# Kernel tuning notes

Hardware: AMD Instinct MI355X
Metric: run time of the kernel (lower is better)

Reference implementation:

```python
import jax, jax.numpy as jnp
import numpy as np

BATCH, SEQ, DIM, HEADS, DSTATE, BLOCK = 2, 4096, 1024, 16, 64, 64
LN_EPS = 1e-6

def segsum(x):
    # x: (..., T) -> (..., T, T); segsum[i, j] = sum_{j < k <= i} x[k]; -inf above diagonal
    T = x.shape[-1]
    cs = jnp.cumsum(x, axis=-1)
    seg = cs[..., :, None] - cs[..., None, :]
    mask = jnp.tril(jnp.ones((T, T), dtype=bool))
    return jnp.where(mask, seg, -jnp.inf)

def ssd_minimal_discrete(X, A, C, B, block_len):
    # X: (b,s,h,p) already multiplied by dt; A: (b,s,h) = A*dt; C readout, B input: (b,s,h,n)
    b, s, h, p = X.shape
    n = B.shape[-1]
    c = s // block_len
    l = block_len
    Xc = X.reshape(b, c, l, h, p)
    Bc = B.reshape(b, c, l, h, n)
    Cc = C.reshape(b, c, l, h, n)
    Ac = A.reshape(b, c, l, h).transpose(0, 3, 1, 2)  # (b,h,c,l)
    A_cumsum = jnp.cumsum(Ac, axis=-1)
    # 1. intra-chunk (diagonal block) outputs
    L = jnp.exp(segsum(Ac))  # (b,h,c,l,l)
    Y_diag = jnp.einsum('bclhn,bcshn,bhcls,bcshp->bclhp', Cc, Bc, L, Xc)
    # 2. states at end of each chunk
    decay_states = jnp.exp(A_cumsum[..., -1:] - A_cumsum)
    states = jnp.einsum('bclhn,bhcl,bclhp->bchpn', Bc, decay_states, Xc)
    # 3. inter-chunk recurrence on chunk states
    init = jnp.zeros_like(states[:, :1])
    states = jnp.concatenate([init, states], axis=1)  # (b,c+1,h,p,n)
    decay_chunk = jnp.exp(segsum(jnp.pad(A_cumsum[..., -1], ((0, 0), (0, 0), (1, 0)))))
    new_states = jnp.einsum('bhzc,bchpn->bzhpn', decay_chunk, states)
    states, final_state = new_states[:, :-1], new_states[:, -1]
    # 4. state -> output contribution (off-diagonal blocks)
    state_decay_out = jnp.exp(A_cumsum)
    Y_off = jnp.einsum('bclhn,bchpn,bhcl->bclhp', Cc, states, state_decay_out)
    return (Y_diag + Y_off).reshape(b, s, h, p), final_state

def setup_inputs():
    key = jax.random.key(0)
    ks = jax.random.split(key, 8)
    X = jax.random.normal(ks[0], (BATCH, SEQ, DIM), jnp.float32)
    B = jax.random.normal(ks[1], (BATCH, SEQ, HEADS * DSTATE), jnp.float32)
    C = jax.random.normal(ks[2], (BATCH, SEQ, HEADS * DSTATE), jnp.float32)
    W_dt = jax.random.normal(ks[3], (DIM, HEADS), jnp.float32) * 0.02
    # dt_bias initializer: inverse-softplus of dt ~ LogUniform(1e-3, 1e-1)
    dt = jnp.exp(jax.random.uniform(ks[4], (1, SEQ, HEADS)) * (jnp.log(0.1) - jnp.log(0.001)) + jnp.log(0.001))
    dt = jnp.clip(dt, 1e-4)
    dt_bias = dt + jnp.log(-jnp.expm1(-dt))
    # a_log initializer: log of Uniform(1, 16)
    a_log = jnp.log(jax.random.uniform(ks[5], (HEADS,), minval=1.0, maxval=16.0))
    W_out = jax.random.normal(ks[6], (DIM, DIM), jnp.float32) * 0.02
    ln_scale = jnp.ones((DIM,), jnp.float32)
    ln_bias = jnp.zeros((DIM,), jnp.float32)
    return {"X": X, "B": B, "C": C, "W_dt": W_dt, "dt_bias": dt_bias, "a_log": a_log,
            "W_out": W_out, "ln_scale": ln_scale, "ln_bias": ln_bias, "block_len": BLOCK}

def reference(X, B, C, W_dt, dt_bias, a_log, W_out, ln_scale, ln_bias, block_len):
    b, s, dim = X.shape
    h = a_log.shape[0]
    Xh = X.reshape(b, s, h, -1)
    Bh = B.reshape(b, s, h, -1)
    Ch = C.reshape(b, s, h, -1)
    dt = jax.nn.softplus(jnp.einsum('bsd,dh->bsh', X, W_dt) + dt_bias)  # (b,s,h)
    A = -jnp.exp(a_log)  # (h,)
    y, final_state = ssd_minimal_discrete(Xh * dt[..., None], A * dt, Ch, Bh, block_len)
    y = y.reshape(b, s, dim)
    mu = jnp.mean(y, axis=-1, keepdims=True)
    var = jnp.mean(jnp.square(y - mu), axis=-1, keepdims=True)
    yn = (y - mu) / jnp.sqrt(var + LN_EPS) * ln_scale + ln_bias
    out = jnp.einsum('bsd,de->bse', yn, W_out)
    return out, final_state
```

## Files before the change

kernel.cpp:

```cpp
#include <hip/hip_runtime.h>
#include <hip/hip_bf16.h>
#include <hip/hip_fp16.h>
#include <math.h>

#define BATCH   2
#define SEQ     4096
#define DIM     1024
#define HEADS   16
#define DSTATE  64
#define HEADDIM 64
#define BLOCKL  64
#define NCHUNK  64
#define ROWS    (BATCH*SEQ)

typedef __attribute__((ext_vector_type(4))) float f32x4;
typedef __attribute__((ext_vector_type(8))) short bf16x8;
typedef __attribute__((ext_vector_type(8))) _Float16 f16x8;

static __device__ __forceinline__ float softplus_f(float x){
    return (x > 20.f) ? x : log1pf(__expf(x));
}
static __device__ __forceinline__ ushort f2b(float f){
    __hip_bfloat16 h = __float2bfloat16(f);
    return *reinterpret_cast<ushort*>(&h);
}
static __device__ __forceinline__ float b2f(ushort u){
    uint x = ((uint)u) << 16;
    return *reinterpret_cast<float*>(&x);
}
static __device__ __forceinline__ void gload16(const void* g, void* l){
    __builtin_amdgcn_global_load_lds((const __attribute__((address_space(1))) unsigned int*)g,
                                     (__attribute__((address_space(3))) unsigned int*)l, 16, 0, 0);
}

__global__ __launch_bounds__(256) void k_dtwt(const float* __restrict__ X,
        const float* __restrict__ Wdt, const float* __restrict__ dtb,
        const float* __restrict__ alog, const float* __restrict__ W,
        float* __restrict__ dt_g, float* __restrict__ dtA_g,
        ushort* __restrict__ Wt){
    __shared__ float xrow[DIM];
    __shared__ float red[16][17];
    __shared__ float t[64][65];
    int bidx = blockIdx.x;
    int tid = threadIdx.x;
    if (bidx < ROWS){
        int r = bidx;
        int s = r & (SEQ-1);
        *(f32x4*)(xrow + tid*4) = *(const f32x4*)(X + (size_t)r*DIM + tid*4);
        __syncthreads();
        int part = tid >> 4, h = tid & 15;
        int d0 = part * 64;
        float acc = 0.f;
        #pragma unroll 8
        for (int i = 0; i < 64; ++i)
            acc += xrow[d0 + i] * Wdt[(size_t)(d0 + i)*HEADS + h];
        red[part][h] = acc;
        __syncthreads();
        if (tid < 16){
            float sum = 0.f;
            #pragma unroll
            for (int p = 0; p < 16; ++p) sum += red[p][tid];
            sum += dtb[(size_t)s*HEADS + tid];
            float dtv = softplus_f(sum);
            dt_g[(size_t)r*HEADS + tid]  = dtv;
            dtA_g[(size_t)r*HEADS + tid] = -__expf(alog[tid]) * dtv;
        }
    } else {
        int bid = bidx - ROWS;
        int kt = bid >> 4, nt = bid & 15;
        int lr = tid >> 4, lc4 = (tid & 15) * 4;
        #pragma unroll
        for (int q = 0; q < 4; ++q){
            int k = lr + q*16;
            *(f32x4*)&t[k][lc4] = *(const f32x4*)(W + (size_t)(kt*64 + k)*DIM + nt*64 + lc4);
        }
        __syncthreads();
        #pragma unroll
        for (int q = 0; q < 4; ++q){
            int n = lr + q*16;
            ushort o[4];
            #pragma unroll
            for (int j = 0; j < 4; ++j) o[j] = f2b(t[lc4+j][n]);
            *(short4*)(Wt + (size_t)(nt*64 + n)*DIM + kt*64 + lc4) = *(short4*)&o[0];
        }
    }
}

__global__ __launch_bounds__(256) void k_chunk(const float* __restrict__ X,
        const float* __restrict__ Bin, const float* __restrict__ Cin,
        const float* __restrict__ dt_g, const float* __restrict__ dtA_g,
        ushort* __restrict__ ybf, ushort* __restrict__ cstate, float* __restrict__ css_g){
    int bid = blockIdx.x;
    int h = bid & 15, c = (bid >> 4) & 63, b = bid >> 10;
    int tid = threadIdx.x;
    int lane = tid & 63, wave = tid >> 6;
    int r0 = b*SEQ + c*BLOCKL;

    __shared__ __align__(16) char region0[18432];
    ushort* Cs  = (ushort*)region0;
    ushort* Bs  = (ushort*)(region0 + 9216);
    ushort* XdT = (ushort*)region0;
    ushort* WBT = (ushort*)(region0 + 9216);
    ushort* Mb  = (ushort*)(region0 + 9216);

    int l  = tid >> 2;
    int c0 = (tid & 3) * 16;

    f32x4 xr[4], br[4], cr[4];
    {
        const float* xp = X   + (size_t)(r0 + l)*DIM + h*HEADDIM + c0;
        const float* bp = Bin + (size_t)(r0 + l)*DIM + h*DSTATE  + c0;
        const float* cp = Cin + (size_t)(r0 + l)*DIM + h*DSTATE  + c0;
        #pragma unroll
        for (int q = 0; q < 4; ++q){
            xr[q] = *(const f32x4*)(xp + q*4);
            br[q] = *(const f32x4*)(bp + q*4);
            cr[q] = *(const f32x4*)(cp + q*4);
        }
    }
    float dt_l = dt_g[(size_t)(r0 + lane)*HEADS + h];
    float a    = dtA_g[(size_t)(r0 + lane)*HEADS + h];
    #pragma unroll
    for (int off = 1; off < 64; off <<= 1){
        float v = __shfl_up(a, off, 64);
        if (lane >= off) a += v;
    }
    float cs63 = __shfl(a, 63, 64);
    float w_l  = __expf(cs63 - a);
    if (tid < 64) css_g[(size_t)bid*64 + tid] = a;

    {
        ushort tc[16], tb[16];
        #pragma unroll
        for (int q = 0; q < 4; ++q)
            #pragma unroll
            for (int j = 0; j < 4; ++j){
                tc[q*4+j] = f2b(cr[q][j]);
                tb[q*4+j] = f2b(br[q][j]);
            }
        *(uint4*)&Cs[l*72 + c0]     = *(uint4*)&tc[0];
        *(uint4*)&Cs[l*72 + c0 + 8] = *(uint4*)&tc[8];
        *(uint4*)&Bs[l*72 + c0]     = *(uint4*)&tb[0];
        *(uint4*)&Bs[l*72 + c0 + 8] = *(uint4*)&tb[8];
    }
    __syncthreads();

    int cl15  = lane & 15;
    int g     = lane >> 4;
    int arow  = wave*16 + cl15;
    int kof   = g * 8;
    int rbase = wave*16 + g*4;

    f32x4 gacc[4];
    #pragma unroll
    for (int j = 0; j < 4; ++j) gacc[j] = (f32x4){0.f,0.f,0.f,0.f};
    #pragma unroll
    for (int k = 0; k < 2; ++k){
        bf16x8 aa = *(const bf16x8*)&Cs[arow*72 + k*32 + kof];
        #pragma unroll
        for (int j = 0; j < 4; ++j){
            bf16x8 bb = *(const bf16x8*)&Bs[(16*j + cl15)*72 + k*32 + kof];
            gacc[j] = __builtin_amdgcn_mfma_f32_16x16x32_bf16(aa, bb, gacc[j], 0, 0, 0);
        }
    }
    __syncthreads();

    {
        float dl = __shfl(dt_l, l, 64);
        float wl = __shfl(w_l,  l, 64);
        #pragma unroll
        for (int q = 0; q < 4; ++q)
            #pragma unroll
            for (int j = 0; j < 4; ++j){
                int p = c0 + q*4 + j;
                XdT[p*72 + l] = f2b(xr[q][j] * dl);
                WBT[p*72 + l] = f2b(br[q][j] * wl);
            }
    }
    __syncthreads();

    f32x4 st[4];
    #pragma unroll
    for (int j = 0; j < 4; ++j) st[j] = (f32x4){0.f,0.f,0.f,0.f};
    #pragma unroll
    for (int k = 0; k < 2; ++k){
        bf16x8 aw = *(const bf16x8*)&XdT[arow*72 + k*32 + kof];
        #pragma unroll
        for (int j = 0; j < 4; ++j){
            bf16x8 bb = *(const bf16x8*)&WBT[(16*j + cl15)*72 + k*32 + kof];
            st[j] = __builtin_amdgcn_mfma_f32_16x16x32_bf16(aw, bb, st[j], 0, 0, 0);
        }
    }
    #pragma unroll
    for (int j = 0; j < 4; ++j)
        #pragma unroll
        for (int r = 0; r < 4; ++r){
            __half hv = __float2half(st[j][r]);
            cstate[(size_t)bid*4096 + (size_t)(rbase + r)*64 + 16*j + cl15] = *(ushort*)&hv;
        }

    float mreg[4][4];
    {
        float csr[4], csc[4];
        #pragma unroll
        for (int r = 0; r < 4; ++r) csr[r] = __shfl(a, rbase + r, 64);
        #pragma unroll
        for (int j = 0; j < 4; ++j) csc[j] = __shfl(a, 16*j + cl15, 64);
        #pragma unroll
        for (int j = 0; j < 4; ++j)
            #pragma unroll
            for (int r = 0; r < 4; ++r){
                int row = rbase + r, col = 16*j + cl15;
                mreg[j][r] = (col <= row) ? gacc[j][r]*__expf(csr[r] - csc[j]) : 0.f;
            }
    }
    __syncthreads();

    #pragma unroll
    for (int j = 0; j < 4; ++j)
        #pragma unroll
        for (int r = 0; r < 4; ++r)
            Mb[(rbase + r)*72 + 16*j + cl15] = f2b(mreg[j][r]);
    __syncthreads();

    f32x4 y[4];
    #pragma unroll
    for (int j = 0; j < 4; ++j) y[j] = (f32x4){0.f,0.f,0.f,0.f};
    #pragma unroll
    for (int k = 0; k < 2; ++k){
        bf16x8 am = *(const bf16x8*)&Mb[arow*72 + k*32 + kof];
        #pragma unroll
        for (int j = 0; j < 4; ++j){
            bf16x8 bx = *(const bf16x8*)&XdT[(16*j + cl15)*72 + k*32 + kof];
            y[j] = __builtin_amdgcn_mfma_f32_16x16x32_bf16(am, bx, y[j], 0, 0, 0);
        }
    }
    #pragma unroll
    for (int j = 0; j < 4; ++j)
        #pragma unroll
        for (int r = 0; r < 4; ++r)
            ybf[(size_t)(r0 + rbase + r)*DIM + h*HEADDIM + 16*j + cl15] = f2b(y[j][r]);
}

__global__ __launch_bounds__(256) void k_scan(ushort* __restrict__ cstate,
        const float* __restrict__ css_g, float* __restrict__ fs_out){
    int bid = blockIdx.x;
    int tile = bid & 7, hh = (bid >> 3) & 15, b = bid >> 7;
    int tid = threadIdx.x;
    int pn = tile*512 + tid*2;
    size_t base0 = (size_t)(b*NCHUNK)*HEADS + hh;
    __shared__ float esh[64];
    if (tid < 64)
        esh[tid] = __expf(css_g[(base0 + (size_t)tid*HEADS)*64 + 63]);
    __syncthreads();
    ushort* p0 = cstate + base0*4096 + pn;
    const size_t cstep = (size_t)HEADS*4096;
    float P0 = 0.f, P1 = 0.f;
    __half2 cur = *(const __half2*)p0;
    __half2 nxt = *(const __half2*)(p0 + cstep);
    for (int c = 0; c < NCHUNK; ++c){
        __half2 fut = nxt;
        if (c + 2 < NCHUNK) fut = *(const __half2*)(p0 + (size_t)(c+2)*cstep);
        *( __half2*)(p0 + (size_t)c*cstep) = __floats2half2_rn(P0, P1);
        float2 cf = __half22float2(cur);
        float e = esh[c];
        P0 = e*P0 + cf.x;
        P1 = e*P1 + cf.y;
        cur = nxt;
        nxt = fut;
    }
    *(float2*)&fs_out[(size_t)(b*HEADS + hh)*4096 + pn] = make_float2(P0, P1);
}

__global__ __launch_bounds__(256) void k_yoff(const float* __restrict__ Cin,
        const ushort* __restrict__ cstate, const float* __restrict__ css_g,
        ushort* __restrict__ ybf){
    int bid = blockIdx.x;
    int h = bid & 15, c = (bid >> 4) & 63, b = bid >> 10;
    int tid = threadIdx.x;
    int lane = tid & 63, wave = tid >> 6;
    int r0 = b*SEQ + c*BLOCKL;
    __shared__ __align__(16) ushort Cs[64*72];
    __shared__ __align__(16) ushort Ss[64*72];
    __shared__ float cse[64];
    {
        int l  = tid >> 2;
        int c0 = (tid & 3) * 16;
        const float* cp = Cin + (size_t)(r0 + l)*DIM + h*DSTATE + c0;
        ushort tc[16];
        #pragma unroll
        for (int q = 0; q < 4; ++q){
            f32x4 vc = *(const f32x4*)(cp + q*4);
            #pragma unroll
            for (int j = 0; j < 4; ++j){
                __half hv = __float2half(vc[j]);
                tc[q*4+j] = *(ushort*)&hv;
            }
        }
        *(uint4*)&Cs[l*72 + c0]     = *(uint4*)&tc[0];
        *(uint4*)&Cs[l*72 + c0 + 8] = *(uint4*)&tc[8];
        const ushort* sp = cstate + (size_t)bid*4096 + (size_t)l*64 + c0;
        *(uint4*)&Ss[l*72 + c0]     = *(const uint4*)sp;
        *(uint4*)&Ss[l*72 + c0 + 8] = *(const uint4*)(sp + 8);
    }
    if (tid < 64) cse[tid] = __expf(css_g[(size_t)bid*64 + tid]);
    __syncthreads();

    int cl15 = lane & 15;
    int g    = lane >> 4;
    int arow = wave*16 + cl15;
    int kof  = g * 8;
    f32x4 acc[4];
    #pragma unroll
    for (int j = 0; j < 4; ++j) acc[j] = (f32x4){0.f,0.f,0.f,0.f};
    #pragma unroll
    for (int k = 0; k < 2; ++k){
        f16x8 a = *(const f16x8*)&Cs[arow*72 + k*32 + kof];
        #pragma unroll
        for (int j = 0; j < 4; ++j){
            f16x8 bb = *(const f16x8*)&Ss[(16*j + cl15)*72 + k*32 + kof];
            acc[j] = __builtin_amdgcn_mfma_f32_16x16x32_f16(a, bb, acc[j], 0, 0, 0);
        }
    }
    int rbase = wave*16 + g*4;
    #pragma unroll
    for (int j = 0; j < 4; ++j)
        #pragma unroll
        for (int r = 0; r < 4; ++r){
            float e = cse[rbase + r];
            size_t idx = (size_t)(r0 + rbase + r)*DIM + h*HEADDIM + 16*j + cl15;
            ybf[idx] = f2b(b2f(ybf[idx]) + e * acc[j][r]);
        }
}

__global__ __launch_bounds__(256) void k_ln(ushort* __restrict__ ybf,
        const float* __restrict__ scale, const float* __restrict__ bias){
    int r = blockIdx.x, tid = threadIdx.x;
    ushort* yp = ybf + (size_t)r*DIM + tid*4;
    short4 raw = *(const short4*)yp;
    float v[4];
    v[0] = b2f((ushort)raw.x); v[1] = b2f((ushort)raw.y);
    v[2] = b2f((ushort)raw.z); v[3] = b2f((ushort)raw.w);
    float s1 = v[0]+v[1]+v[2]+v[3];
    float s2 = v[0]*v[0]+v[1]*v[1]+v[2]*v[2]+v[3]*v[3];
    #pragma unroll
    for (int m = 32; m > 0; m >>= 1){
        s1 += __shfl_xor(s1, m, 64);
        s2 += __shfl_xor(s2, m, 64);
    }
    __shared__ float w1[4], w2[4];
    int wv = tid >> 6;
    if ((tid & 63) == 0){ w1[wv] = s1; w2[wv] = s2; }
    __syncthreads();
    float S1 = w1[0]+w1[1]+w1[2]+w1[3];
    float S2 = w2[0]+w2[1]+w2[2]+w2[3];
    float mu  = S1 * (1.f/DIM);
    float var = S2 * (1.f/DIM) - mu*mu;
    float rstd = rsqrtf(var + 1e-6f);
    int d = tid*4;
    f32x4 sc = *(const f32x4*)(scale + d);
    f32x4 bi = *(const f32x4*)(bias + d);
    ushort o[4];
    #pragma unroll
    for (int j = 0; j < 4; ++j)
        o[j] = f2b((v[j] - mu)*rstd*sc[j] + bi[j]);
    *(short4*)yp = *(short4*)&o[0];
}

__global__ __launch_bounds__(256) void k_gemm(const ushort* __restrict__ A,
        const ushort* __restrict__ Bt, float* __restrict__ Out){
    __shared__ __align__(16) ushort As[128*32];
    __shared__ __align__(16) ushort Bsh[128*32];
    int bid = blockIdx.x;
    int wgid = (bid & 7)*64 + (bid >> 3);
    int bn = wgid & 7, bm = wgid >> 3;
    int tid = threadIdx.x;
    int lane = tid & 63, wave = tid >> 6;
    int wr = wave >> 1, wc = wave & 1;
    f32x4 acc[4][4];
    #pragma unroll
    for (int i = 0; i < 4; ++i)
        #pragma unroll
        for (int j = 0; j < 4; ++j)
            acc[i][j] = (f32x4){0.f, 0.f, 0.f, 0.f};
    const ushort* Ag = A  + (size_t)bm*128*1024;
    const ushort* Bg = Bt + (size_t)bn*128*1024;
    int row0 = tid >> 2;
    int col0 = (tid & 3) * 8;
    for (int k0 = 0; k0 < 1024; k0 += 32){
        const ushort* sA = Ag + (size_t)row0*1024 + k0 + col0;
        const ushort* sB = Bg + (size_t)row0*1024 + k0 + col0;
        gload16(sA,           &As[row0*32 + col0]);
        gload16(sA + 64*1024, &As[(row0+64)*32 + col0]);
        gload16(sB,           &Bsh[row0*32 + col0]);
        gload16(sB + 64*1024, &Bsh[(row0+64)*32 + col0]);
        __syncthreads();
        bf16x8 af[4], bfr[4];
        #pragma unroll
        for (int i = 0; i < 4; ++i){
            int arow = wr*64 + i*16 + (lane & 15);
            af[i] = *(const bf16x8*)&As[arow*32 + ((lane >> 4) << 3)];
        }
        #pragma unroll
        for (int j = 0; j < 4; ++j){
            int brow = wc*64 + j*16 + (lane & 15);
            bfr[j] = *(const bf16x8*)&Bsh[brow*32 + ((lane >> 4) << 3)];
        }
        #pragma unroll
        for (int i = 0; i < 4; ++i)
            #pragma unroll
            for (int j = 0; j < 4; ++j)
                acc[i][j] = __builtin_amdgcn_mfma_f32_16x16x32_bf16(af[i], bfr[j], acc[i][j], 0, 0, 0);
        __syncthreads();
    }
    #pragma unroll
    for (int i = 0; i < 4; ++i){
        int m0 = bm*128 + wr*64 + i*16 + ((lane >> 4) << 2);
        #pragma unroll
        for (int j = 0; j < 4; ++j){
            int n = bn*128 + wc*64 + j*16 + (lane & 15);
            #pragma unroll
            for (int reg = 0; reg < 4; ++reg)
                Out[(size_t)(m0 + reg)*1024 + n] = acc[i][j][reg];
        }
    }
}

extern "C" void kernel_launch(void* const* d_in, const int* in_sizes, int n_in,
                              void* d_out, int out_size, void* d_ws, size_t ws_size,
                              hipStream_t stream){
    const float* X    = (const float*)d_in[0];
    const float* Bin  = (const float*)d_in[1];
    const float* Cin  = (const float*)d_in[2];
    const float* Wdt  = (const float*)d_in[3];
    const float* dtb  = (const float*)d_in[4];
    const float* alog = (const float*)d_in[5];
    const float* Wout = (const float*)d_in[6];
    const float* lns  = (const float*)d_in[7];
    const float* lnb  = (const float*)d_in[8];

    float* out = (float*)d_out;
    float* fs_out = out + (size_t)ROWS*DIM;

    char* ws = (char*)d_ws;
    float*  dt_g   = (float*)(ws);
    float*  dtA_g  = (float*)(ws + 524288);
    float*  css_g  = (float*)(ws + 1048576);
    ushort* cstate = (ushort*)(ws + 1572864);
    ushort* ybf    = (ushort*)(ws + 18350080);
    ushort* Wt     = (ushort*)(ws + 35127296);

    k_dtwt <<<ROWS + 256,         256, 0, stream>>>(X, Wdt, dtb, alog, Wout, dt_g, dtA_g, Wt);
    k_chunk<<<BATCH*NCHUNK*HEADS, 256, 0, stream>>>(X, Bin, Cin, dt_g, dtA_g, ybf, cstate, css_g);
    k_scan <<<BATCH*HEADS*8,      256, 0, stream>>>(cstate, css_g, fs_out);
    k_yoff <<<BATCH*NCHUNK*HEADS, 256, 0, stream>>>(Cin, cstate, css_g, ybf);
    k_ln   <<<ROWS,               256, 0, stream>>>(ybf, lns, lnb);
    k_gemm <<<512,                256, 0, stream>>>(ybf, Wt, out);
}
```

Before: 122.7 us.

## Fuse LayerNorm into output GEMM A-tile load

Removes the standalone LayerNorm kernel. The GEMM now computes per-row mean and rstd for its 128-row A tile in a prologue and normalizes A elements on the fly while staging them into shared memory. This saves one kernel launch and a full read+write pass over the bf16 activations. In exchange, each of the 8 column blocks recomputes the row statistics, which re-reads A, and the A load becomes a register path instead of a direct global-to-LDS load. The result also changes slightly because of when bf16 rounding happens.

Result: slower. 150.4 us (+22.6%).

```diff
diff --git a/kernel.cpp b/kernel.cpp
--- a/kernel.cpp
+++ b/kernel.cpp
@@ -333,67 +333,89 @@
         }
 }
 
-__global__ __launch_bounds__(256) void k_ln(ushort* __restrict__ ybf,
-        const float* __restrict__ scale, const float* __restrict__ bias){
-    int r = blockIdx.x, tid = threadIdx.x;
-    ushort* yp = ybf + (size_t)r*DIM + tid*4;
-    short4 raw = *(const short4*)yp;
-    float v[4];
-    v[0] = b2f((ushort)raw.x); v[1] = b2f((ushort)raw.y);
-    v[2] = b2f((ushort)raw.z); v[3] = b2f((ushort)raw.w);
-    float s1 = v[0]+v[1]+v[2]+v[3];
-    float s2 = v[0]*v[0]+v[1]*v[1]+v[2]*v[2]+v[3]*v[3];
-    #pragma unroll
-    for (int m = 32; m > 0; m >>= 1){
-        s1 += __shfl_xor(s1, m, 64);
-        s2 += __shfl_xor(s2, m, 64);
-    }
-    __shared__ float w1[4], w2[4];
-    int wv = tid >> 6;
-    if ((tid & 63) == 0){ w1[wv] = s1; w2[wv] = s2; }
-    __syncthreads();
-    float S1 = w1[0]+w1[1]+w1[2]+w1[3];
-    float S2 = w2[0]+w2[1]+w2[2]+w2[3];
-    float mu  = S1 * (1.f/DIM);
-    float var = S2 * (1.f/DIM) - mu*mu;
-    float rstd = rsqrtf(var + 1e-6f);
-    int d = tid*4;
-    f32x4 sc = *(const f32x4*)(scale + d);
-    f32x4 bi = *(const f32x4*)(bias + d);
-    ushort o[4];
-    #pragma unroll
-    for (int j = 0; j < 4; ++j)
-        o[j] = f2b((v[j] - mu)*rstd*sc[j] + bi[j]);
-    *(short4*)yp = *(short4*)&o[0];
-}
-
 __global__ __launch_bounds__(256) void k_gemm(const ushort* __restrict__ A,
-        const ushort* __restrict__ Bt, float* __restrict__ Out){
+        const ushort* __restrict__ Bt, const float* __restrict__ lns,
+        const float* __restrict__ lnb, float* __restrict__ Out){
     __shared__ __align__(16) ushort As[128*32];
     __shared__ __align__(16) ushort Bsh[128*32];
+    __shared__ float2 mursh[128];
+    __shared__ float scs[1024];
+    __shared__ float bis[1024];
     int bid = blockIdx.x;
     int wgid = (bid & 7)*64 + (bid >> 3);
     int bn = wgid & 7, bm = wgid >> 3;
     int tid = threadIdx.x;
     int lane = tid & 63, wave = tid >> 6;
     int wr = wave >> 1, wc = wave & 1;
+    const ushort* Ag = A  + (size_t)bm*128*1024;
+    const ushort* Bg = Bt + (size_t)bn*128*1024;
+
+    *(f32x4*)&scs[tid*4] = *(const f32x4*)(lns + tid*4);
+    *(f32x4*)&bis[tid*4] = *(const f32x4*)(lnb + tid*4);
+    {
+        float ps1[8], ps2[8];
+        #pragma unroll
+        for (int it = 0; it < 8; ++it){
+            int row = it*16 + (tid >> 4);
+            const ushort* rp = Ag + (size_t)row*1024 + (tid & 15)*8;
+            float s1 = 0.f, s2 = 0.f;
+            #pragma unroll
+            for (int q = 0; q < 8; ++q){
+                uint4 v = *(const uint4*)(rp + q*128);
+                const ushort* pv = (const ushort*)&v;
+                #pragma unroll
+                for (int e = 0; e < 8; ++e){
+                    float f = b2f(pv[e]);
+                    s1 += f; s2 += f*f;
+                }
+            }
+            ps1[it] = s1; ps2[it] = s2;
+        }
+        #pragma unroll
+        for (int it = 0; it < 8; ++it){
+            #pragma unroll
+            for (int m = 1; m < 16; m <<= 1){
+                ps1[it] += __shfl_xor(ps1[it], m, 64);
+                ps2[it] += __shfl_xor(ps2[it], m, 64);
+            }
+            if ((tid & 15) == 0){
+                int row = it*16 + (tid >> 4);
+                float mu  = ps1[it] * (1.f/DIM);
+                float var = ps2[it] * (1.f/DIM) - mu*mu;
+                mursh[row] = make_float2(mu, rsqrtf(var + 1e-6f));
+            }
+        }
+    }
+    __syncthreads();
+
     f32x4 acc[4][4];
     #pragma unroll
     for (int i = 0; i < 4; ++i)
         #pragma unroll
         for (int j = 0; j < 4; ++j)
             acc[i][j] = (f32x4){0.f, 0.f, 0.f, 0.f};
-    const ushort* Ag = A  + (size_t)bm*128*1024;
-    const ushort* Bg = Bt + (size_t)bn*128*1024;
     int row0 = tid >> 2;
     int col0 = (tid & 3) * 8;
     for (int k0 = 0; k0 < 1024; k0 += 32){
-        const ushort* sA = Ag + (size_t)row0*1024 + k0 + col0;
-        const ushort* sB = Bg + (size_t)row0*1024 + k0 + col0;
-        gload16(sA,           &As[row0*32 + col0]);
-        gload16(sA + 64*1024, &As[(row0+64)*32 + col0]);
-        gload16(sB,           &Bsh[row0*32 + col0]);
-        gload16(sB + 64*1024, &Bsh[(row0+64)*32 + col0]);
+        f32x4 sc0 = *(f32x4*)&scs[k0 + col0];
+        f32x4 sc1 = *(f32x4*)&scs[k0 + col0 + 4];
+        f32x4 bi0 = *(f32x4*)&bis[k0 + col0];
+        f32x4 bi1 = *(f32x4*)&bis[k0 + col0 + 4];
+        #pragma unroll
+        for (int pass = 0; pass < 2; ++pass){
+            int row = row0 + pass*64;
+            uint4 v = *(const uint4*)(Ag + (size_t)row*1024 + k0 + col0);
+            float2 mr = mursh[row];
+            const ushort* pv = (const ushort*)&v;
+            ushort o[8];
+            #pragma unroll
+            for (int j = 0; j < 4; ++j){
+                o[j]   = f2b((b2f(pv[j])   - mr.x)*mr.y*sc0[j] + bi0[j]);
+                o[j+4] = f2b((b2f(pv[j+4]) - mr.x)*mr.y*sc1[j] + bi1[j]);
+            }
+            *(uint4*)&As[row*32 + col0] = *(uint4*)&o[0];
+            gload16(Bg + (size_t)row*1024 + k0 + col0, &Bsh[row*32 + col0]);
+        }
         __syncthreads();
         bf16x8 af[4], bfr[4];
         #pragma unroll
@@ -454,6 +476,5 @@
     k_chunk<<<BATCH*NCHUNK*HEADS, 256, 0, stream>>>(X, Bin, Cin, dt_g, dtA_g, ybf, cstate, css_g);
     k_scan <<<BATCH*HEADS*8,      256, 0, stream>>>(cstate, css_g, fs_out);
     k_yoff <<<BATCH*NCHUNK*HEADS, 256, 0, stream>>>(Cin, cstate, css_g, ybf);
-    k_ln   <<<ROWS,               256, 0, stream>>>(ybf, lns, lnb);
-    k_gemm <<<512,                256, 0, stream>>>(ybf, Wt, out);
-}
+    k_gemm <<<512,                256, 0, stream>>>(ybf, Wt, lns, lnb, out);
+}
```
